# Performance work log

Hardware: AMD Instinct MI355X
Metric: run time of the kernel (lower is better)

The kernel has to match this reference:

```python
import jax, jax.numpy as jnp
import numpy as np

FP8_MAX = 448.0  # e4m3 max
SCALE_MARGIN = 0.8


def _fp8_quant_dequant(t, scale):
    # scaled value is <= 448*0.8 by construction, so no saturation/overflow
    q = (t / scale).astype(jnp.float8_e4m3fn)
    return q.astype(jnp.float32) * scale


def setup_inputs() -> dict:
    key = jax.random.key(0)
    k1, k2 = jax.random.split(key)
    B, S, D_IN, D_OUT = 4, 2048, 2048, 2048
    x = jax.random.normal(k1, (B, S, D_IN), dtype=jnp.float32)
    weight = jax.random.normal(k2, (D_OUT, D_IN), dtype=jnp.float32)
    bias = jnp.zeros((D_OUT,), dtype=jnp.float32)
    return {"x": x, "weight": weight, "bias": bias}


def reference(x, weight, bias):
    # Shared FP8ScalingManager: amax history = [amax_x] for x, then [amax_x, amax_w] for w.
    amax_x = jnp.max(jnp.abs(x))
    amax_w = jnp.max(jnp.abs(weight))
    x_scale = amax_x / (FP8_MAX * SCALE_MARGIN)
    w_scale = jnp.maximum(amax_x, amax_w) / (FP8_MAX * SCALE_MARGIN)  # history max
    x_scale = jax.lax.stop_gradient(x_scale)  # .item() detaches in torch
    w_scale = jax.lax.stop_gradient(w_scale)
    # quantize to fp8 e4m3, dequantize, scaled matmul (math of torch._scaled_mm)
    x_dq = _fp8_quant_dequant(x, x_scale)      # [B,S,Din]
    w_dq = _fp8_quant_dequant(weight, w_scale)  # [Dout,Din]
    out = jnp.einsum('bsd,od->bso', x_dq, w_dq)  # [B,S,Dout]
    return out + bias
```

## Files before the change

### kernel.cpp

```cpp
#include <hip/hip_runtime.h>
#include <stdint.h>

typedef float v4f __attribute__((ext_vector_type(4)));

#define FP8_DENOM 358.4f


__device__ __forceinline__ unsigned pack4_fp8(float a, float b, float c, float d) {
  int v = 0;
  v = __builtin_amdgcn_cvt_pk_fp8_f32(a, b, v, false);
  v = __builtin_amdgcn_cvt_pk_fp8_f32(c, d, v, true);
  return (unsigned)v;
}

__device__ __forceinline__ void gload_lds16(const void* g, void* l) {
  __builtin_amdgcn_global_load_lds(
      (const __attribute__((address_space(1))) uint32_t*)(uintptr_t)g,
      (__attribute__((address_space(3))) uint32_t*)(uint32_t)(uintptr_t)l,
      16, 0, 0);
}


__global__ void amax_kernel(const float4* __restrict__ p, int n4, unsigned* __restrict__ out) {
  float m = 0.f;
  const int stride = gridDim.x * blockDim.x;
  for (int i = blockIdx.x * blockDim.x + threadIdx.x; i < n4; i += stride) {
    float4 v = p[i];
    m = fmaxf(m, fmaxf(fmaxf(fabsf(v.x), fabsf(v.y)), fmaxf(fabsf(v.z), fabsf(v.w))));
  }
#pragma unroll
  for (int off = 32; off > 0; off >>= 1)
    m = fmaxf(m, __shfl_down(m, off, 64));
  __shared__ float red[4];
  const int lane = threadIdx.x & 63, wid = threadIdx.x >> 6;
  if (lane == 0) red[wid] = m;
  __syncthreads();
  if (threadIdx.x == 0) {
    float mm = fmaxf(fmaxf(red[0], red[1]), fmaxf(red[2], red[3]));
    atomicMax(out, __float_as_uint(mm));
  }
}


__global__ void quant_kernel(const float4* __restrict__ in, uint4* __restrict__ outq,
                             int n16, const unsigned* __restrict__ amax, int which) {
  const float ax = __uint_as_float(amax[0]);
  const float aw = __uint_as_float(amax[1]);
  const float scale = (which == 0) ? (ax / FP8_DENOM) : (fmaxf(ax, aw) / FP8_DENOM);
  const int stride = gridDim.x * blockDim.x;
  for (int i = blockIdx.x * blockDim.x + threadIdx.x; i < n16; i += stride) {
    float4 v0 = in[4 * i + 0], v1 = in[4 * i + 1], v2 = in[4 * i + 2], v3 = in[4 * i + 3];
    uint4 r;
    r.x = pack4_fp8(v0.x / scale, v0.y / scale, v0.z / scale, v0.w / scale);
    r.y = pack4_fp8(v1.x / scale, v1.y / scale, v1.z / scale, v1.w / scale);
    r.z = pack4_fp8(v2.x / scale, v2.y / scale, v2.z / scale, v2.w / scale);
    r.w = pack4_fp8(v3.x / scale, v3.y / scale, v3.z / scale, v3.w / scale);
    outq[i] = r;
  }
}


__global__ void __launch_bounds__(256) gemm_fp8(
    const uint8_t* __restrict__ Aq, const uint8_t* __restrict__ Bq,
    const float* __restrict__ bias, float* __restrict__ out,
    const unsigned* __restrict__ amax) {
  constexpr int K = 2048, N = 2048, BK = 64;
  __shared__ alignas(16) uint8_t sA[128 * BK];
  __shared__ alignas(16) uint8_t sB[128 * BK];

  const int tid = threadIdx.x;
  const int lane = tid & 63;
  const int wid = tid >> 6;
  const int wy = wid >> 1, wx = wid & 1;
  const long tileM = (long)blockIdx.y * 128;
  const long tileN = (long)blockIdx.x * 128;

  v4f acc[4][4];
#pragma unroll
  for (int i = 0; i < 4; ++i)
#pragma unroll
    for (int j = 0; j < 4; ++j) acc[i][j] = (v4f)(0.f);

  const int sr = tid >> 2;
  const int sc = tid & 3;
  const int scc = sc ^ ((sr >> 2) & 3);
  const uint8_t* gA0 = Aq + (tileM + sr) * K + scc * 16;
  const uint8_t* gA1 = gA0 + 64L * K;
  const uint8_t* gB0 = Bq + (tileN + sr) * K + scc * 16;
  const uint8_t* gB1 = gB0 + 64L * K;

  const int q = lane >> 4;
  const int mrow = lane & 15;
  const int sig = (lane >> 2) & 3;

  for (int k0 = 0; k0 < K; k0 += BK) {
    gload_lds16(gA0 + k0, sA + tid * 16);
    gload_lds16(gA1 + k0, sA + 4096 + tid * 16);
    gload_lds16(gB0 + k0, sB + tid * 16);
    gload_lds16(gB1 + k0, sB + 4096 + tid * 16);
    __syncthreads();

    long af[2][4], bf[2][4];
#pragma unroll
    for (int s = 0; s < 2; ++s) {
      const int phys = 16 * ((s * 2 + (q >> 1)) ^ sig) + (q & 1) * 8;
#pragma unroll
      for (int i = 0; i < 4; ++i) {
        af[s][i] = *(const long*)(sA + (wy * 64 + i * 16 + mrow) * 64 + phys);
        bf[s][i] = *(const long*)(sB + (wx * 64 + i * 16 + mrow) * 64 + phys);
      }
    }
#pragma unroll
    for (int s = 0; s < 2; ++s)
#pragma unroll
      for (int i = 0; i < 4; ++i)
#pragma unroll
        for (int j = 0; j < 4; ++j)
          acc[i][j] = __builtin_amdgcn_mfma_f32_16x16x32_fp8_fp8(af[s][i], bf[s][j],
                                                                 acc[i][j], 0, 0, 0);
    __syncthreads();
  }

  const float ax = __uint_as_float(amax[0]);
  const float aw = __uint_as_float(amax[1]);
  const float scale = (ax / FP8_DENOM) * (fmaxf(ax, aw) / FP8_DENOM);
#pragma unroll
  for (int j = 0; j < 4; ++j) {
    const long col = tileN + wx * 64 + j * 16 + mrow;
    const float bv = bias[col];
#pragma unroll
    for (int i = 0; i < 4; ++i) {
      const long row = tileM + wy * 64 + i * 16 + q * 4;
#pragma unroll
      for (int r = 0; r < 4; ++r)
        out[(row + r) * N + col] = acc[i][j][r] * scale + bv;
    }
  }
}


extern "C" void kernel_launch(void* const* d_in, const int* in_sizes, int n_in,
                              void* d_out, int out_size, void* d_ws, size_t ws_size,
                              hipStream_t stream) {
  const float* x = (const float*)d_in[0];
  const float* w = (const float*)d_in[1];
  const float* bias = (const float*)d_in[2];
  float* out = (float*)d_out;

  const int M = 8192, N = 2048, K = 2048;
  const long nx = (long)M * K, nw = (long)N * K;

  unsigned* amax = (unsigned*)d_ws;
  uint8_t* xq = (uint8_t*)d_ws + 256;
  uint8_t* wq = xq + nx;

  hipMemsetAsync(d_ws, 0, 8, stream);

  amax_kernel<<<1024, 256, 0, stream>>>((const float4*)x, (int)(nx / 4), amax + 0);
  amax_kernel<<<512, 256, 0, stream>>>((const float4*)w, (int)(nw / 4), amax + 1);

  quant_kernel<<<4096, 256, 0, stream>>>((const float4*)x, (uint4*)xq, (int)(nx / 16), amax, 0);
  quant_kernel<<<1024, 256, 0, stream>>>((const float4*)w, (uint4*)wq, (int)(nw / 16), amax, 1);

  gemm_fp8<<<dim3(N / 128, M / 128), 256, 0, stream>>>(xq, wq, bias, out, amax);
}
```

Measured before the change: 216.5 us.

## Use 16x16x128 scaled MFMA with BK=128 and merge amax/quant launches

Replaces the fp8 16x16x32 MFMA with the MI355X scaled 16x16x128 f8f6f4 MFMA using unit scales (0x7F), and doubles the K tile to 128 with a new XOR swizzle and 16-byte LDS fragment loads. The x and weight amax kernels are merged into one launch, as are the two quant kernels, to cut launch count and tail effects. This halves main-loop iterations and the MFMA instruction count, at the cost of twice the LDS footprint per block, which may lower occupancy.

```diff
diff --git a/kernel.cpp b/kernel.cpp
--- a/kernel.cpp
+++ b/kernel.cpp
@@ -2,6 +2,7 @@
 #include <stdint.h>
 
 typedef float v4f __attribute__((ext_vector_type(4)));
+typedef int v8i __attribute__((ext_vector_type(8)));
 
 #define FP8_DENOM 358.4f
 
@@ -21,10 +22,17 @@
 }
 
 
-__global__ void amax_kernel(const float4* __restrict__ p, int n4, unsigned* __restrict__ out) {
+__global__ void amax2_kernel(const float4* __restrict__ x, int nx4,
+                             const float4* __restrict__ w, int nw4,
+                             int xblocks, unsigned* __restrict__ out) {
+  const int isw = ((int)blockIdx.x >= xblocks) ? 1 : 0;
+  const float4* p = isw ? w : x;
+  const int n4 = isw ? nw4 : nx4;
+  const int b0 = isw ? ((int)blockIdx.x - xblocks) : (int)blockIdx.x;
+  const int nb = isw ? ((int)gridDim.x - xblocks) : xblocks;
   float m = 0.f;
-  const int stride = gridDim.x * blockDim.x;
-  for (int i = blockIdx.x * blockDim.x + threadIdx.x; i < n4; i += stride) {
+  const long stride = (long)nb * blockDim.x;
+  for (long i = (long)b0 * blockDim.x + threadIdx.x; i < n4; i += stride) {
     float4 v = p[i];
     m = fmaxf(m, fmaxf(fmaxf(fabsf(v.x), fabsf(v.y)), fmaxf(fabsf(v.z), fabsf(v.w))));
   }
@@ -32,23 +40,30 @@
   for (int off = 32; off > 0; off >>= 1)
     m = fmaxf(m, __shfl_down(m, off, 64));
   __shared__ float red[4];
-  const int lane = threadIdx.x & 63, wid = threadIdx.x >> 6;
-  if (lane == 0) red[wid] = m;
+  const int lane = threadIdx.x & 63, wvid = threadIdx.x >> 6;
+  if (lane == 0) red[wvid] = m;
   __syncthreads();
   if (threadIdx.x == 0) {
     float mm = fmaxf(fmaxf(red[0], red[1]), fmaxf(red[2], red[3]));
-    atomicMax(out, __float_as_uint(mm));
+    atomicMax(out + isw, __float_as_uint(mm));
   }
 }
 
 
-__global__ void quant_kernel(const float4* __restrict__ in, uint4* __restrict__ outq,
-                             int n16, const unsigned* __restrict__ amax, int which) {
+__global__ void quant2_kernel(const float4* __restrict__ x, uint4* __restrict__ xq, int nx16,
+                              const float4* __restrict__ w, uint4* __restrict__ wq, int nw16,
+                              int xblocks, const unsigned* __restrict__ amax) {
   const float ax = __uint_as_float(amax[0]);
   const float aw = __uint_as_float(amax[1]);
-  const float scale = (which == 0) ? (ax / FP8_DENOM) : (fmaxf(ax, aw) / FP8_DENOM);
-  const int stride = gridDim.x * blockDim.x;
-  for (int i = blockIdx.x * blockDim.x + threadIdx.x; i < n16; i += stride) {
+  const int isw = ((int)blockIdx.x >= xblocks) ? 1 : 0;
+  const float scale = isw ? (fmaxf(ax, aw) / FP8_DENOM) : (ax / FP8_DENOM);
+  const float4* in = isw ? w : x;
+  uint4* outq = isw ? wq : xq;
+  const int n16 = isw ? nw16 : nx16;
+  const int b0 = isw ? ((int)blockIdx.x - xblocks) : (int)blockIdx.x;
+  const int nb = isw ? ((int)gridDim.x - xblocks) : xblocks;
+  const long stride = (long)nb * blockDim.x;
+  for (long i = (long)b0 * blockDim.x + threadIdx.x; i < n16; i += stride) {
     float4 v0 = in[4 * i + 0], v1 = in[4 * i + 1], v2 = in[4 * i + 2], v3 = in[4 * i + 3];
     uint4 r;
     r.x = pack4_fp8(v0.x / scale, v0.y / scale, v0.z / scale, v0.w / scale);
@@ -60,11 +75,11 @@
 }
 
 
-__global__ void __launch_bounds__(256) gemm_fp8(
+__global__ void __launch_bounds__(256) gemm_mx(
     const uint8_t* __restrict__ Aq, const uint8_t* __restrict__ Bq,
     const float* __restrict__ bias, float* __restrict__ out,
     const unsigned* __restrict__ amax) {
-  constexpr int K = 2048, N = 2048, BK = 64;
+  constexpr int K = 2048, N = 2048, BK = 128;
   __shared__ alignas(16) uint8_t sA[128 * BK];
   __shared__ alignas(16) uint8_t sB[128 * BK];
 
@@ -81,43 +96,49 @@
 #pragma unroll
     for (int j = 0; j < 4; ++j) acc[i][j] = (v4f)(0.f);
 
-  const int sr = tid >> 2;
-  const int sc = tid & 3;
-  const int scc = sc ^ ((sr >> 2) & 3);
-  const uint8_t* gA0 = Aq + (tileM + sr) * K + scc * 16;
-  const uint8_t* gA1 = gA0 + 64L * K;
-  const uint8_t* gB0 = Bq + (tileN + sr) * K + scc * 16;
-  const uint8_t* gB1 = gB0 + 64L * K;
+  const int srow = tid >> 3;
+  const int schunk = (tid & 7) ^ (srow & 7);
+  const uint8_t* gA = Aq + (tileM + srow) * K + schunk * 16;
+  const uint8_t* gB = Bq + (tileN + srow) * K + schunk * 16;
 
   const int q = lane >> 4;
   const int mrow = lane & 15;
-  const int sig = (lane >> 2) & 3;
+
+  int aoff[4][2], boff[4][2];
+#pragma unroll
+  for (int i = 0; i < 4; ++i) {
+    const int rA = wy * 64 + i * 16 + mrow, swA = rA & 7;
+    aoff[i][0] = rA * 128 + 16 * ((2 * q) ^ swA);
+    aoff[i][1] = rA * 128 + 16 * ((2 * q + 1) ^ swA);
+    const int rB = wx * 64 + i * 16 + mrow, swB = rB & 7;
+    boff[i][0] = rB * 128 + 16 * ((2 * q) ^ swB);
+    boff[i][1] = rB * 128 + 16 * ((2 * q + 1) ^ swB);
+  }
 
   for (int k0 = 0; k0 < K; k0 += BK) {
-    gload_lds16(gA0 + k0, sA + tid * 16);
-    gload_lds16(gA1 + k0, sA + 4096 + tid * 16);
-    gload_lds16(gB0 + k0, sB + tid * 16);
-    gload_lds16(gB1 + k0, sB + 4096 + tid * 16);
+#pragma unroll
+    for (int s = 0; s < 4; ++s) {
+      gload_lds16(gA + (long)s * 32 * K + k0, sA + s * 4096 + tid * 16);
+      gload_lds16(gB + (long)s * 32 * K + k0, sB + s * 4096 + tid * 16);
+    }
     __syncthreads();
 
-    long af[2][4], bf[2][4];
+    union Frag { v8i v; uint4 h[2]; };
+    Frag a[4], b[4];
 #pragma unroll
-    for (int s = 0; s < 2; ++s) {
-      const int phys = 16 * ((s * 2 + (q >> 1)) ^ sig) + (q & 1) * 8;
-#pragma unroll
-      for (int i = 0; i < 4; ++i) {
-        af[s][i] = *(const long*)(sA + (wy * 64 + i * 16 + mrow) * 64 + phys);
-        bf[s][i] = *(const long*)(sB + (wx * 64 + i * 16 + mrow) * 64 + phys);
-      }
+    for (int i = 0; i < 4; ++i) {
+      a[i].h[0] = *(const uint4*)(sA + aoff[i][0]);
+      a[i].h[1] = *(const uint4*)(sA + aoff[i][1]);
+      b[i].h[0] = *(const uint4*)(sB + boff[i][0]);
+      b[i].h[1] = *(const uint4*)(sB + boff[i][1]);
     }
 #pragma unroll
-    for (int s = 0; s < 2; ++s)
+    for (int i = 0; i < 4; ++i)
 #pragma unroll
-      for (int i = 0; i < 4; ++i)
-#pragma unroll
-        for (int j = 0; j < 4; ++j)
-          acc[i][j] = __builtin_amdgcn_mfma_f32_16x16x32_fp8_fp8(af[s][i], bf[s][j],
-                                                                 acc[i][j], 0, 0, 0);
+      for (int j = 0; j < 4; ++j)
+        acc[i][j] = __builtin_amdgcn_mfma_scale_f32_16x16x128_f8f6f4(
+            a[i].v, b[j].v, acc[i][j],  0,  0,
+             0, 0x7F7F7F7F,  0, 0x7F7F7F7F);
     __syncthreads();
   }
 
@@ -156,11 +177,10 @@
 
   hipMemsetAsync(d_ws, 0, 8, stream);
 
-  amax_kernel<<<1024, 256, 0, stream>>>((const float4*)x, (int)(nx / 4), amax + 0);
-  amax_kernel<<<512, 256, 0, stream>>>((const float4*)w, (int)(nw / 4), amax + 1);
-
-  quant_kernel<<<4096, 256, 0, stream>>>((const float4*)x, (uint4*)xq, (int)(nx / 16), amax, 0);
-  quant_kernel<<<1024, 256, 0, stream>>>((const float4*)w, (uint4*)wq, (int)(nw / 16), amax, 1);
-
-  gemm_fp8<<<dim3(N / 128, M / 128), 256, 0, stream>>>(xq, wq, bias, out, amax);
+  amax2_kernel<<<4096, 256, 0, stream>>>((const float4*)x, (int)(nx / 4),
+                                         (const float4*)w, (int)(nw / 4), 3072, amax);
+  quant2_kernel<<<5120, 256, 0, stream>>>((const float4*)x, (uint4*)xq, (int)(nx / 16),
+                                          (const float4*)w, (uint4*)wq, (int)(nw / 16),
+                                          4096, amax);
+  gemm_mx<<<dim3(N / 128, M / 128), 256, 0, stream>>>(xq, wq, bias, out, amax);
 }
```

Measured after the change: 213.7 us. No clear change (-1.3%).
